# Kernel tuning notes

Measured on AMD Instinct MI355X. Metric: run time of the kernel, lower is better.

The kernel has to match this reference:

```python
import jax, jax.numpy as jnp
import numpy as np

H, W = 101, 31
HEADS, DH, FREQ = 8, 64, 64
C_DIM = 256
INNER = HEADS * DH
EPS = 1e-5


def _conv2d(x, w, b):
    # x: (B, Cin, H, W), w: (Cout, Cin, 3, 3) -> SAME padding, stride 1
    y = jax.lax.conv_general_dilated(x, w, (1, 1), 'SAME',
                                     dimension_numbers=('NCHW', 'OIHW', 'NCHW'))
    return y + b[None, :, None, None]


def setup_inputs() -> dict:
    key = jax.random.key(0)
    ks = jax.random.split(key, 8)
    B = 32
    N = H * W  # 3131
    s = 0.02
    x = jax.random.normal(ks[0], (B, N, C_DIM), jnp.float32)
    conv_fx_w = jax.random.normal(ks[1], (INNER, C_DIM, 3, 3), jnp.float32) * s
    conv_fx_b = jnp.zeros((INNER,), jnp.float32)
    conv_x_w = jax.random.normal(ks[2], (INNER, C_DIM, 3, 3), jnp.float32) * s
    conv_x_b = jnp.zeros((INNER,), jnp.float32)
    gate_w = jax.random.normal(ks[3], (FREQ, DH), jnp.float32) * s  # nn.Linear weight (out,in)
    gate_b = jnp.zeros((FREQ,), jnp.float32)
    temperature = jnp.full((1, HEADS, 1, 1), 0.5, jnp.float32)
    ln_gamma = jnp.ones((FREQ, DH), jnp.float32)
    ln_beta = jnp.zeros((FREQ, DH), jnp.float32)
    mlp_w = jax.random.normal(ks[4], (DH, DH), jnp.float32) * s
    out_w = jax.random.normal(ks[5], (C_DIM, INNER), jnp.float32) * s
    out_b = jnp.zeros((C_DIM,), jnp.float32)
    # fixed (non-trainable) spectral basis, L2-normalized per row like F.normalize(dim=-1)
    inver = jax.random.normal(ks[6], (N, FREQ), jnp.float32)
    inver = inver / jnp.linalg.norm(inver, axis=-1, keepdims=True)
    return dict(x=x, conv_fx_w=conv_fx_w, conv_fx_b=conv_fx_b, conv_x_w=conv_x_w,
                conv_x_b=conv_x_b, gate_w=gate_w, gate_b=gate_b,
                temperature=temperature, ln_gamma=ln_gamma, ln_beta=ln_beta,
                mlp_w=mlp_w, out_w=out_w, out_b=out_b, inver=inver)


def reference(x, conv_fx_w, conv_fx_b, conv_x_w, conv_x_b, gate_w, gate_b,
              temperature, ln_gamma, ln_beta, mlp_w, out_w, out_b, inver):
    B, N, C = x.shape
    xi = x.reshape(B, H, W, C).transpose(0, 3, 1, 2)  # (B, C, H, W)

    def proj(w, b):
        y = _conv2d(xi, w, b)                                  # (B, inner, H, W)
        return y.transpose(0, 2, 3, 1).reshape(B, N, HEADS, DH).transpose(0, 2, 1, 3)  # (B,h,N,d)

    fx_mid = proj(conv_fx_w, conv_fx_b)
    x_mid = proj(conv_x_w, conv_x_b)

    temp = jnp.clip(temperature, 0.1, 5.0)                      # (1,h,1,1)
    logits = jnp.einsum('bhnc,gc->bhng', x_mid, gate_w) + gate_b
    gate = jax.nn.softmax(logits / temp, axis=-1)               # (B,h,N,g)
    eigens = gate * inver[None, None]                           # (B,h,N,g)

    spec = jnp.einsum('bhnc,bhng->bhgc', fx_mid, eigens)        # (B,h,g,c)
    # LayerNorm over the trailing (g, c) axes jointly
    mu = spec.mean(axis=(-2, -1), keepdims=True)
    var = spec.var(axis=(-2, -1), keepdims=True)
    spec = (spec - mu) * jax.lax.rsqrt(var + EPS) * ln_gamma + ln_beta

    out_spec = jnp.einsum('bhgi,io->bhgo', spec, mlp_w)
    out_x = jnp.einsum('bhgc,bhng->bhnc', out_spec, eigens)     # (B,h,N,c)
    out_x = out_x.transpose(0, 2, 1, 3).reshape(B, N, HEADS * DH)
    return jnp.einsum('bnd,cd->bnc', out_x, out_w) + out_b      # to_out (dropout is identity)
```

## Files before the change

kernel.cpp:

```cpp
#include <hip/hip_runtime.h>
#include <hip/hip_bf16.h>
#include <stdint.h>

#define HH 101
#define WW 31
#define NN 3131
#define NPAD 3136
#define BB 32
#define NH 8
#define CDIM 256
#define GG 64
#define HP 103
#define WP 33

typedef __attribute__((ext_vector_type(8))) short bf16x8;
typedef __attribute__((ext_vector_type(4))) float f32x4;
typedef __attribute__((ext_vector_type(4))) unsigned short ushort4_t;
typedef __attribute__((ext_vector_type(8))) unsigned short ushort8_t;
typedef __attribute__((ext_vector_type(4))) float float4_t;

static __device__ __forceinline__ unsigned short f2bf(float f) {
  union { float f; uint32_t u; } v; v.f = f;
  uint32_t u = v.u;
  return (unsigned short)((u + 0x7fffu + ((u >> 16) & 1u)) >> 16);
}
static __device__ __forceinline__ float bf2f(unsigned short h) {
  union { uint32_t u; float f; } v; v.u = ((uint32_t)h) << 16;
  return v.f;
}
static __device__ __forceinline__ void gload_lds16(const void* g, void* l) {
  __builtin_amdgcn_global_load_lds((const __attribute__((address_space(1))) void*)g,
                                   (__attribute__((address_space(3))) void*)l, 16, 0, 0);
}
static __device__ __forceinline__ int xcd_swz(int bid, int nwg) {
  int q = nwg >> 3, r = nwg & 7;
  int xcd = bid & 7, pos = bid >> 3;
  int base = (xcd < r) ? xcd * (q + 1) : r * (q + 1) + (xcd - r) * q;
  return base + pos;
}

__global__ void k_pad(const float* __restrict__ x, unsigned short* __restrict__ xpad, int b0) {
  const int xx = blockIdx.x, yy = blockIdx.y, b = blockIdx.z;
  const int t = threadIdx.x;
  ushort4_t o; o.x = 0; o.y = 0; o.z = 0; o.w = 0;
  if (yy >= 1 && yy <= HH && xx >= 1 && xx <= WW) {
    const int n = (yy - 1) * WW + (xx - 1);
    const float4_t v = *(const float4_t*)(x + (((int64_t)(b0 + b) * NN + n) * CDIM + t * 4));
    o.x = f2bf(v.x); o.y = f2bf(v.y); o.z = f2bf(v.z); o.w = f2bf(v.w);
  }
  *(ushort4_t*)(xpad + (((int64_t)b * HP + yy) * WP + xx) * CDIM + t * 4) = o;
}

__global__ void k_wpack(const float* __restrict__ fxw, const float* __restrict__ xw,
                        const float* __restrict__ fxb, const float* __restrict__ xb,
                        const float* __restrict__ gw,
                        unsigned short* __restrict__ Wb, float* __restrict__ bias,
                        unsigned short* __restrict__ gwb) {
  int tid = blockIdx.x * blockDim.x + threadIdx.x;
  const int total = 9 * 1024 * 256;
  if (tid < total) {
    int cin = tid & 255; int rest = tid >> 8; int co = rest & 1023; int t = rest >> 10;
    float v = (co < 512) ? fxw[(int64_t)co * 2304 + cin * 9 + t]
                         : xw[(int64_t)(co - 512) * 2304 + cin * 9 + t];
    Wb[tid] = f2bf(v);
  }
  if (tid < 1024) bias[tid] = (tid < 512) ? fxb[tid] : xb[tid - 512];
  if (tid < 4096) gwb[tid] = f2bf(gw[tid]);
}

__global__ void k_pprep(const float* __restrict__ mlp, const float* __restrict__ outw,
                        unsigned short* __restrict__ Pt) {
  int h = blockIdx.x >> 6, i = blockIdx.x & 63, co = threadIdx.x;
  float a = 0.f;
  for (int c = 0; c < 64; ++c) a += mlp[i * 64 + c] * outw[(int64_t)co * 512 + h * 64 + c];
  Pt[((int64_t)h * 256 + co) * 64 + i] = f2bf(a);
}

__global__ void k_padzero(unsigned short* __restrict__ fxT, unsigned short* __restrict__ xmid,
                          int CB) {
  int tid = blockIdx.x * blockDim.x + threadIdx.x;
  if (tid >= CB * 2560) return;
  {
    int j = tid % 5; int rc = tid / 5;
    fxT[(int64_t)rc * NPAD + NN + j] = 0;
  }
  {
    int d = tid & 63; int rest = tid >> 6;
    int j = rest % 5; int bh = rest / 5;
    xmid[((int64_t)bh * NPAD + NN + j) * 64 + d] = 0;
  }
}

static __device__ __forceinline__ void stage_a8(const unsigned short* aS0, const unsigned short* aS1,
                                                unsigned short* lds, int s, int wid, int kt) {
  const int t = kt >> 3;
  const int dy = (t >= 6) + (t >= 3);
  const int dx = t - dy * 3;
  const int aoff = (dy * WP + dx) * CDIM + (kt & 7) * 32;
  gload_lds16(aS0 + aoff, lds + s * 16384 + wid * 512);
  gload_lds16(aS1 + aoff, lds + s * 16384 + 4096 + wid * 512);
}
static __device__ __forceinline__ void stage_b8(const unsigned short* bS0, const unsigned short* bS1,
                                                unsigned short* lds, int s, int wid, int kt) {
  const int t = kt >> 3;
  const int boff = t * (1024 * CDIM) + (kt & 7) * 32;
  gload_lds16(bS0 + boff, lds + s * 16384 + 8192 + wid * 512);
  gload_lds16(bS1 + boff, lds + s * 16384 + 8192 + 4096 + wid * 512);
}

__launch_bounds__(512, 2)
__global__ void k_conv8(const unsigned short* __restrict__ xpad,
                        const unsigned short* __restrict__ Wb,
                        const float* __restrict__ bias,
                        unsigned short* __restrict__ fxT,
                        unsigned short* __restrict__ xmid) {
  extern __shared__ unsigned short lds[];
  const int swz = xcd_swz(blockIdx.x, gridDim.x);
  const int r   = swz % 52;
  const int b   = swz / 52;
  const int bx  = r & 3;
  const int mt  = r >> 2;
  const int tid = threadIdx.x, wid = tid >> 6, lane = tid & 63;
  const int wm = wid >> 2, wn = wid & 3;
  const int arow = lane & 15, col16 = lane >> 4;
  const int n00 = mt * 256, co00 = bx * 256;

  const int srow = wid * 16 + (lane >> 2);
  const int tc   = ((lane & 3) ^ ((srow ^ (srow >> 2)) & 3)) * 8;
  int na0 = n00 + srow;        if (na0 >= NN) na0 = NN - 1;
  int na1 = n00 + srow + 128;  if (na1 >= NN) na1 = NN - 1;
  const int y0 = na0 / WW, x0v = na0 % WW;
  const int y1 = na1 / WW, x1v = na1 % WW;
  const unsigned short* aS0 = xpad + ((int64_t)(b * HP + y0) * WP + x0v) * CDIM + tc;
  const unsigned short* aS1 = xpad + ((int64_t)(b * HP + y1) * WP + x1v) * CDIM + tc;
  const unsigned short* bS0 = Wb + (int64_t)(co00 + srow) * CDIM + tc;
  const unsigned short* bS1 = Wb + (int64_t)(co00 + srow + 128) * CDIM + tc;

  const int rdcol = (col16 ^ ((arow ^ (arow >> 2)) & 3)) * 8;

  f32x4 acc[8][4] = {};

  stage_a8(aS0, aS1, lds, 0, wid, 0); stage_b8(bS0, bS1, lds, 0, wid, 0);
  stage_a8(aS0, aS1, lds, 1, wid, 1); stage_b8(bS0, bS1, lds, 1, wid, 1);

  for (int kt = 0; kt < 72; ++kt) {
    const int s = kt & 3;
    const unsigned short* sA = lds + s * 16384;
    const unsigned short* sB = sA + 8192;
    const int s2  = (kt + 2) & 3;
    const int kt2 = (kt + 2 > 71) ? 71 : kt + 2;

    asm volatile("s_waitcnt vmcnt(4)" ::: "memory");
    __builtin_amdgcn_s_barrier();
    asm volatile("" ::: "memory");
    __builtin_amdgcn_sched_barrier(0);

    stage_a8(aS0, aS1, lds, s2, wid, kt2);
    stage_b8(bS0, bS1, lds, s2, wid, kt2);

    bf16x8 av[8], bv[4];
    #pragma unroll
    for (int mf = 0; mf < 8; ++mf)
      av[mf] = *(const bf16x8*)(sA + (wm * 128 + mf * 16 + arow) * 32 + rdcol);
    #pragma unroll
    for (int nf = 0; nf < 4; ++nf)
      bv[nf] = *(const bf16x8*)(sB + (wn * 64 + nf * 16 + arow) * 32 + rdcol);
    __builtin_amdgcn_s_setprio(1);
    #pragma unroll
    for (int mf = 0; mf < 8; ++mf)
      #pragma unroll
      for (int nf = 0; nf < 4; ++nf)
        acc[mf][nf] = __builtin_amdgcn_mfma_f32_16x16x32_bf16(av[mf], bv[nf], acc[mf][nf], 0, 0, 0);
    __builtin_amdgcn_s_setprio(0);
  }

  asm volatile("s_waitcnt vmcnt(0)" ::: "memory");

  const int rowoff = col16 * 4;
  #pragma unroll
  for (int mf = 0; mf < 8; ++mf) {
    const int nr = n00 + wm * 128 + mf * 16 + rowoff;
    #pragma unroll
    for (int nf = 0; nf < 4; ++nf) {
      const int co = co00 + wn * 64 + nf * 16 + arow;
      const float bvs = bias[co];
      const float v0 = acc[mf][nf][0] + bvs;
      const float v1 = acc[mf][nf][1] + bvs;
      const float v2 = acc[mf][nf][2] + bvs;
      const float v3 = acc[mf][nf][3] + bvs;
      if (bx < 2) {
        const int h = co >> 6, c = co & 63;
        unsigned short* dst = fxT + ((int64_t)((b * NH + h) * 64 + c)) * NPAD + nr;
        if (nr + 3 < NN) {
          ushort4_t o; o.x = f2bf(v0); o.y = f2bf(v1); o.z = f2bf(v2); o.w = f2bf(v3);
          *(ushort4_t*)dst = o;
        } else {
          if (nr + 0 < NN) dst[0] = f2bf(v0);
          if (nr + 1 < NN) dst[1] = f2bf(v1);
          if (nr + 2 < NN) dst[2] = f2bf(v2);
          if (nr + 3 < NN) dst[3] = f2bf(v3);
        }
      } else {
        const int h = (co >> 6) & 7, d = co & 63;
        unsigned short* dst = xmid + ((int64_t)(b * NH + h) * NPAD + nr) * 64 + d;
        if (nr + 0 < NN) dst[0] = f2bf(v0);
        if (nr + 1 < NN) dst[64] = f2bf(v1);
        if (nr + 2 < NN) dst[128] = f2bf(v2);
        if (nr + 3 < NN) dst[192] = f2bf(v3);
      }
    }
  }
}

__global__ void k_eig(const unsigned short* __restrict__ xmid,
                      const unsigned short* __restrict__ gwb,
                      const float* __restrict__ gateb,
                      const float* __restrict__ temperature,
                      const float* __restrict__ inver,
                      unsigned short* __restrict__ eigT,
                      unsigned short* __restrict__ eigN) {
  __shared__ unsigned short egN[64 * 72];
  __shared__ unsigned short egT[64 * 72];
  const int nt = blockIdx.x, h = blockIdx.y, b = blockIdx.z;
  const int tid = threadIdx.x;
  const int w = tid >> 6, lane = tid & 63;
  const int n0 = nt * 64 + w * 16;
  const int bh = b * NH + h;
  float tv = temperature[h];
  tv = fminf(fmaxf(tv, 0.1f), 5.0f);
  const float itemp = 1.0f / tv;
  const int arow = lane & 15;
  const int koff = (lane >> 4) * 8;
  const unsigned short* aptr = xmid + ((int64_t)bh * NPAD + (n0 + arow)) * 64 + koff;
  bf16x8 a0 = *(const bf16x8*)(aptr);
  bf16x8 a1 = *(const bf16x8*)(aptr + 32);
  f32x4 acc[4] = {};
  #pragma unroll
  for (int ng = 0; ng < 4; ++ng) {
    const unsigned short* bptr = gwb + (ng * 16 + arow) * 64 + koff;
    bf16x8 b0 = *(const bf16x8*)(bptr);
    bf16x8 b1 = *(const bf16x8*)(bptr + 32);
    acc[ng] = __builtin_amdgcn_mfma_f32_16x16x32_bf16(a0, b0, acc[ng], 0, 0, 0);
    acc[ng] = __builtin_amdgcn_mfma_f32_16x16x32_bf16(a1, b1, acc[ng], 0, 0, 0);
  }
  #pragma unroll
  for (int r = 0; r < 4; ++r) {
    const int nl = w * 16 + ((lane >> 4) << 2) + r;
    const int n = nt * 64 + nl;
    float vals[4];
    #pragma unroll
    for (int ng = 0; ng < 4; ++ng) vals[ng] = (acc[ng][r] + gateb[ng * 16 + arow]) * itemp;
    float mx = fmaxf(fmaxf(vals[0], vals[1]), fmaxf(vals[2], vals[3]));
    #pragma unroll
    for (int s = 1; s < 16; s <<= 1) mx = fmaxf(mx, __shfl_xor(mx, s));
    float ex[4]; float sum = 0.f;
    #pragma unroll
    for (int ng = 0; ng < 4; ++ng) { ex[ng] = __expf(vals[ng] - mx); sum += ex[ng]; }
    #pragma unroll
    for (int s = 1; s < 16; s <<= 1) sum += __shfl_xor(sum, s);
    const float inv = 1.0f / sum;
    const bool valid = (n < NN);
    #pragma unroll
    for (int ng = 0; ng < 4; ++ng) {
      const int g = ng * 16 + arow;
      float iv = valid ? inver[(int64_t)n * GG + g] : 0.f;
      unsigned short u = valid ? f2bf(ex[ng] * inv * iv) : (unsigned short)0;
      egN[nl * 72 + g] = u;
      egT[g * 72 + nl] = u;
    }
  }
  __syncthreads();
  const int row = tid >> 2, c0 = (tid & 3) << 4;
  {
    ushort8_t v0 = *(ushort8_t*)&egN[row * 72 + c0];
    ushort8_t v1 = *(ushort8_t*)&egN[row * 72 + c0 + 8];
    unsigned short* dst = eigN + ((int64_t)bh * NPAD + nt * 64 + row) * 64 + c0;
    *(ushort8_t*)dst = v0; *(ushort8_t*)(dst + 8) = v1;
  }
  {
    ushort8_t v0 = *(ushort8_t*)&egT[row * 72 + c0];
    ushort8_t v1 = *(ushort8_t*)&egT[row * 72 + c0 + 8];
    unsigned short* dst = eigT + ((int64_t)(bh * 64 + row)) * NPAD + nt * 64 + c0;
    *(ushort8_t*)dst = v0; *(ushort8_t*)(dst + 8) = v1;
  }
}

__launch_bounds__(256, 1)
__global__ void k_specln(const unsigned short* __restrict__ eigT,
                         const unsigned short* __restrict__ fxT,
                         const float* __restrict__ gamma, const float* __restrict__ beta,
                         const unsigned short* __restrict__ Pt,
                         unsigned short* __restrict__ m2t) {
  extern __shared__ char sm[];
  float* sacc = (float*)sm;
  unsigned short* specb = (unsigned short*)(sm + 66560);
  float* red = (float*)(sm + 74752);
  unsigned short* mstrip = (unsigned short*)(sm + 74784);
  const int bhl = blockIdx.x;
  const int h = bhl & 7, bl = bhl >> 3;
  const int tid = threadIdx.x, w = tid >> 6, lane = tid & 63;
  const int arow = lane & 15, col16 = lane >> 4;
  const int koff = col16 * 8;
  const unsigned short* eb = eigT + (int64_t)bhl * 64 * NPAD;
  const unsigned short* fb = fxT + (int64_t)bhl * 64 * NPAD;

  const int ks0 = (98 * w) >> 2, ks1 = (98 * (w + 1)) >> 2;
  f32x4 acc[4][4] = {};
  for (int ks = ks0; ks < ks1; ++ks) {
    const int k0 = ks * 32 + koff;
    bf16x8 av[4], bv[4];
    #pragma unroll
    for (int mg = 0; mg < 4; ++mg) av[mg] = *(const bf16x8*)(eb + (int64_t)(mg * 16 + arow) * NPAD + k0);
    #pragma unroll
    for (int ng = 0; ng < 4; ++ng) bv[ng] = *(const bf16x8*)(fb + (int64_t)(ng * 16 + arow) * NPAD + k0);
    #pragma unroll
    for (int mg = 0; mg < 4; ++mg)
      #pragma unroll
      for (int ng = 0; ng < 4; ++ng)
        acc[mg][ng] = __builtin_amdgcn_mfma_f32_16x16x32_bf16(av[mg], bv[ng], acc[mg][ng], 0, 0, 0);
  }
  float* pw = sacc + w * (64 * 65);
  #pragma unroll
  for (int mg = 0; mg < 4; ++mg)
    #pragma unroll
    for (int ng = 0; ng < 4; ++ng)
      #pragma unroll
      for (int r = 0; r < 4; ++r)
        pw[(mg * 16 + col16 * 4 + r) * 65 + ng * 16 + arow] = acc[mg][ng][r];
  __syncthreads();

  float vloc[16];
  float lsum = 0.f, lsq = 0.f;
  #pragma unroll
  for (int idx = 0; idx < 16; ++idx) {
    const int e = tid + idx * 256;
    const int g = e >> 6, c = e & 63;
    float v = sacc[g * 65 + c] + sacc[4160 + g * 65 + c] +
              sacc[8320 + g * 65 + c] + sacc[12480 + g * 65 + c];
    vloc[idx] = v; lsum += v; lsq += v * v;
  }
  #pragma unroll
  for (int s = 1; s < 64; s <<= 1) { lsum += __shfl_xor(lsum, s); lsq += __shfl_xor(lsq, s); }
  if (lane == 0) { red[w] = lsum; red[4 + w] = lsq; }
  __syncthreads();
  const float tsum = red[0] + red[1] + red[2] + red[3];
  const float tsq = red[4] + red[5] + red[6] + red[7];
  const float mu = tsum * (1.0f / 4096.0f);
  const float var = tsq * (1.0f / 4096.0f) - mu * mu;
  const float rs = rsqrtf(var + 1e-5f);
  #pragma unroll
  for (int idx = 0; idx < 16; ++idx) {
    const int e = tid + idx * 256;
    const int g = e >> 6, c = e & 63;
    float sv = (vloc[idx] - mu) * rs * gamma[e] + beta[e];
    specb[g * 64 + ((((c >> 3) ^ (g & 7))) << 3) + (c & 7)] = f2bf(sv);
  }
  __syncthreads();

  f32x4 a2[4][4] = {};
  const unsigned short* pth = Pt + ((int64_t)h * 256 + w * 64) * 64;
  #pragma unroll
  for (int kk = 0; kk < 2; ++kk) {
    const int i0 = kk * 32 + koff;
    const int i8 = (i0 >> 3);
    bf16x8 av2[4], bv2[4];
    #pragma unroll
    for (int mg = 0; mg < 4; ++mg) {
      const int g = mg * 16 + arow;
      av2[mg] = *(const bf16x8*)(specb + g * 64 + ((i8 ^ (g & 7)) << 3));
    }
    #pragma unroll
    for (int ng = 0; ng < 4; ++ng)
      bv2[ng] = *(const bf16x8*)(pth + (ng * 16 + arow) * 64 + i0);
    #pragma unroll
    for (int mg = 0; mg < 4; ++mg)
      #pragma unroll
      for (int ng = 0; ng < 4; ++ng)
        a2[mg][ng] = __builtin_amdgcn_mfma_f32_16x16x32_bf16(av2[mg], bv2[ng], a2[mg][ng], 0, 0, 0);
  }
  unsigned short* ms = mstrip + w * (64 * 72);
  #pragma unroll
  for (int mg = 0; mg < 4; ++mg)
    #pragma unroll
    for (int ng = 0; ng < 4; ++ng)
      #pragma unroll
      for (int r = 0; r < 4; ++r)
        ms[(ng * 16 + arow) * 72 + mg * 16 + col16 * 4 + r] = f2bf(a2[mg][ng][r]);
  __syncthreads();
  #pragma unroll
  for (int e0 = 0; e0 < 8; ++e0) {
    const int e = lane + e0 * 64;
    const int row = e >> 3, g8 = e & 7;
    ushort8_t v = *(ushort8_t*)&ms[row * 72 + g8 * 8];
    *(ushort8_t*)(m2t + ((int64_t)(bl * 256 + w * 64 + row)) * 512 + h * 64 + g8 * 8) = v;
  }
}

__launch_bounds__(256)
__global__ void k_out(const unsigned short* __restrict__ eigN,
                      const unsigned short* __restrict__ m2t,
                      const float* __restrict__ outb,
                      float* __restrict__ out, int b0) {
  const int swz = xcd_swz(blockIdx.x, gridDim.x);
  const int ct = swz & 1;
  const int mt = (swz >> 1) % 25;
  const int b  = swz / 50;
  const int w = threadIdx.x >> 6, lane = threadIdx.x & 63;
  const int wm = w >> 1, wn = w & 1;
  const int arow = lane & 15, koff = (lane >> 4) * 8;
  const int co0 = ct * 128 + wn * 64;
  const int n0 = mt * 128 + wm * 64;
  f32x4 acc[4][4] = {};
  const unsigned short* ebase = eigN + (int64_t)b * NH * NPAD * 64;
  const unsigned short* mbase = m2t + (int64_t)b * 256 * 512;
  for (int ks = 0; ks < 16; ++ks) {
    const int hh = ks >> 1;
    const int g0 = (ks & 1) * 32 + koff;
    bf16x8 av[4], bv[4];
    #pragma unroll
    for (int mg = 0; mg < 4; ++mg) {
      int n = n0 + mg * 16 + arow;
      if (n > NPAD - 1) n = NPAD - 1;
      av[mg] = *(const bf16x8*)(ebase + ((int64_t)hh * NPAD + n) * 64 + g0);
    }
    #pragma unroll
    for (int ng = 0; ng < 4; ++ng)
      bv[ng] = *(const bf16x8*)(mbase + (int64_t)(co0 + ng * 16 + arow) * 512 + ks * 32 + koff);
    #pragma unroll
    for (int mg = 0; mg < 4; ++mg)
      #pragma unroll
      for (int ng = 0; ng < 4; ++ng)
        acc[mg][ng] = __builtin_amdgcn_mfma_f32_16x16x32_bf16(av[mg], bv[ng], acc[mg][ng], 0, 0, 0);
  }
  #pragma unroll
  for (int mg = 0; mg < 4; ++mg) {
    const int nr = n0 + mg * 16 + ((lane >> 4) << 2);
    #pragma unroll
    for (int ng = 0; ng < 4; ++ng) {
      const int co = co0 + ng * 16 + arow;
      const float bv = outb[co];
      #pragma unroll
      for (int r = 0; r < 4; ++r) {
        if (nr + r < NN)
          out[((int64_t)(b0 + b) * NN + nr + r) * 256 + co] = acc[mg][ng][r] + bv;
      }
    }
  }
}

extern "C" void kernel_launch(void* const* d_in, const int* in_sizes, int n_in,
                              void* d_out, int out_size, void* d_ws, size_t ws_size,
                              hipStream_t stream) {
  const float* x     = (const float*)d_in[0];
  const float* fxw   = (const float*)d_in[1];
  const float* fxb   = (const float*)d_in[2];
  const float* xw    = (const float*)d_in[3];
  const float* xb    = (const float*)d_in[4];
  const float* gw    = (const float*)d_in[5];
  const float* gb    = (const float*)d_in[6];
  const float* temp  = (const float*)d_in[7];
  const float* gamma = (const float*)d_in[8];
  const float* beta  = (const float*)d_in[9];
  const float* mlp   = (const float*)d_in[10];
  const float* outw  = (const float*)d_in[11];
  const float* outb  = (const float*)d_in[12];
  const float* inver = (const float*)d_in[13];
  float* out = (float*)d_out;
  char* ws = (char*)d_ws;
  (void)in_sizes; (void)n_in; (void)out_size;

  hipFuncSetAttribute(reinterpret_cast<const void*>(k_conv8),
                      hipFuncAttributeMaxDynamicSharedMemorySize, 131072);
  hipFuncSetAttribute(reinterpret_cast<const void*>(k_specln),
                      hipFuncAttributeMaxDynamicSharedMemorySize, 131072);

  int CB = 1;
  {
    const int cands[6] = {32, 16, 8, 4, 2, 1};
    for (int i = 0; i < 6; ++i) {
      unsigned long long need = 4993024ull + (unsigned long long)cands[i] * 14847488ull;
      if (need <= (unsigned long long)ws_size) { CB = cands[i]; break; }
    }
  }

  unsigned short* Wb   = (unsigned short*)(ws + 0);
  float*          bias = (float*)(ws + 4718592);
  unsigned short* gwb  = (unsigned short*)(ws + 4722688);
  unsigned short* Pt   = (unsigned short*)(ws + 4730880);
  const size_t F0      = 4993024;
  const size_t szXpad  = (size_t)CB * 1740288;
  const size_t szM2t   = (size_t)CB * 262144;
  const size_t szBig   = (size_t)CB * 3211264;
  unsigned short* xpad = (unsigned short*)(ws + F0);
  unsigned short* m2t  = (unsigned short*)(ws + F0 + szXpad);
  unsigned short* fxT  = (unsigned short*)(ws + F0 + szXpad + szM2t);
  unsigned short* xmid = (unsigned short*)(ws + F0 + szXpad + szM2t + szBig);
  unsigned short* eigT = (unsigned short*)(ws + F0 + szXpad + szM2t + 2 * szBig);
  unsigned short* eigN = (unsigned short*)(ws + F0 + szXpad + szM2t + 3 * szBig);

  k_wpack<<<dim3(9216), dim3(256), 0, stream>>>(fxw, xw, fxb, xb, gw, Wb, bias, gwb);
  k_pprep<<<dim3(512), dim3(256), 0, stream>>>(mlp, outw, Pt);

  for (int b0 = 0; b0 < BB; b0 += CB) {
    k_pad<<<dim3(WP, HP, CB), dim3(64), 0, stream>>>(x, xpad, b0);
    k_padzero<<<dim3(CB * 10), dim3(256), 0, stream>>>(fxT, xmid, CB);
    k_conv8<<<dim3(52 * CB), dim3(512), 131072, stream>>>(xpad, Wb, bias, fxT, xmid);
    k_eig<<<dim3(49, 8, CB), dim3(256), 0, stream>>>(xmid, gwb, gb, temp, inver, eigT, eigN);
    k_specln<<<dim3(CB * 8), dim3(256), 111648, stream>>>(eigT, fxT, gamma, beta, Pt, m2t);
    k_out<<<dim3(50 * CB), dim3(256), 0, stream>>>(eigN, m2t, outb, out, b0);
  }
}
```

Measured before the change: 930.1 us.

## Restructure conv GEMM main loop into double-buffered 64-wide K steps with interleaved phases

Rewrites the implicit-GEMM conv main loop from a 4-stage ring of 32-wide K tiles into a 2-buffer scheme where each iteration covers 64 K elements, split into four phases that interleave LDS reads, global-to-LDS prefetch of the next tile, barriers and MFMA pairs. The LDS swizzle pattern also changes. The aim is to cut barrier count per K element and to overlap memory prefetch with MFMA work more finely in a ping-pong style. In exchange, the per-buffer LDS footprint and barrier count per iteration go up, and the new swizzle may be less effective at avoiding bank conflicts.

```diff
diff --git a/kernel.cpp b/kernel.cpp
--- a/kernel.cpp
+++ b/kernel.cpp
@@ -89,23 +89,6 @@
     int j = rest % 5; int bh = rest / 5;
     xmid[((int64_t)bh * NPAD + NN + j) * 64 + d] = 0;
   }
-}
-
-static __device__ __forceinline__ void stage_a8(const unsigned short* aS0, const unsigned short* aS1,
-                                                unsigned short* lds, int s, int wid, int kt) {
-  const int t = kt >> 3;
-  const int dy = (t >= 6) + (t >= 3);
-  const int dx = t - dy * 3;
-  const int aoff = (dy * WP + dx) * CDIM + (kt & 7) * 32;
-  gload_lds16(aS0 + aoff, lds + s * 16384 + wid * 512);
-  gload_lds16(aS1 + aoff, lds + s * 16384 + 4096 + wid * 512);
-}
-static __device__ __forceinline__ void stage_b8(const unsigned short* bS0, const unsigned short* bS1,
-                                                unsigned short* lds, int s, int wid, int kt) {
-  const int t = kt >> 3;
-  const int boff = t * (1024 * CDIM) + (kt & 7) * 32;
-  gload_lds16(bS0 + boff, lds + s * 16384 + 8192 + wid * 512);
-  gload_lds16(bS1 + boff, lds + s * 16384 + 8192 + 4096 + wid * 512);
 }
 
 __launch_bounds__(512, 2)
@@ -126,7 +109,7 @@
   const int n00 = mt * 256, co00 = bx * 256;
 
   const int srow = wid * 16 + (lane >> 2);
-  const int tc   = ((lane & 3) ^ ((srow ^ (srow >> 2)) & 3)) * 8;
+  const int tc   = ((lane & 3) ^ ((lane >> 3) & 3)) * 8;
   int na0 = n00 + srow;        if (na0 >= NN) na0 = NN - 1;
   int na1 = n00 + srow + 128;  if (na1 >= NN) na1 = NN - 1;
   const int y0 = na0 / WW, x0v = na0 % WW;
@@ -136,42 +119,96 @@
   const unsigned short* bS0 = Wb + (int64_t)(co00 + srow) * CDIM + tc;
   const unsigned short* bS1 = Wb + (int64_t)(co00 + srow + 128) * CDIM + tc;
 
-  const int rdcol = (col16 ^ ((arow ^ (arow >> 2)) & 3)) * 8;
+  const int rdsz = (col16 ^ ((arow >> 1) & 3)) * 8;
 
   f32x4 acc[8][4] = {};
 
-  stage_a8(aS0, aS1, lds, 0, wid, 0); stage_b8(bS0, bS1, lds, 0, wid, 0);
-  stage_a8(aS0, aS1, lds, 1, wid, 1); stage_b8(bS0, bS1, lds, 1, wid, 1);
-
-  for (int kt = 0; kt < 72; ++kt) {
-    const int s = kt & 3;
-    const unsigned short* sA = lds + s * 16384;
-    const unsigned short* sB = sA + 8192;
-    const int s2  = (kt + 2) & 3;
-    const int kt2 = (kt + 2 > 71) ? 71 : kt + 2;
-
+#define STAGE_A(s, kk, aoffv)                                        \
+  { unsigned short* d = lds + (s) * 32768 + (kk) * 8192 + wid * 512; \
+    gload_lds16(aS0 + (aoffv) + (kk) * 32, d);                       \
+    gload_lds16(aS1 + (aoffv) + (kk) * 32, d + 4096); }
+#define STAGE_B(s, kk, boffv)                                                \
+  { unsigned short* d = lds + (s) * 32768 + 16384 + (kk) * 8192 + wid * 512; \
+    gload_lds16(bS0 + (boffv) + (kk) * 32, d);                               \
+    gload_lds16(bS1 + (boffv) + (kk) * 32, d + 4096); }
+#define KOFF(ks, aoffv, boffv)                              \
+  { const int tap = (ks) >> 2;                              \
+    const int dy = (tap >= 6) + (tap >= 3);                 \
+    const int dx = tap - dy * 3;                            \
+    const int cb = ((ks) & 3) << 6;                         \
+    aoffv = (dy * WP + dx) * CDIM + cb;                     \
+    boffv = tap * 262144 + cb; }
+
+  int aoff0, boff0;
+  KOFF(0, aoff0, boff0);
+  STAGE_A(0, 0, aoff0); STAGE_B(0, 0, boff0);
+  STAGE_A(0, 1, aoff0); STAGE_B(0, 1, boff0);
+  asm volatile("s_waitcnt vmcnt(4)" ::: "memory");
+  __builtin_amdgcn_s_barrier();
+  asm volatile("" ::: "memory");
+
+#define MFMA_PAIR(n0i, n1i)                                                              \
+  __builtin_amdgcn_s_setprio(1);                                                        \
+  _Pragma("unroll")                                                                      \
+  for (int mf = 0; mf < 8; ++mf) {                                                       \
+    acc[mf][n0i] = __builtin_amdgcn_mfma_f32_16x16x32_bf16(av[mf], bv0, acc[mf][n0i], 0, 0, 0); \
+    acc[mf][n1i] = __builtin_amdgcn_mfma_f32_16x16x32_bf16(av[mf], bv1, acc[mf][n1i], 0, 0, 0); \
+  }                                                                                      \
+  __builtin_amdgcn_s_setprio(0);
+#define BAR_PRE()                                              \
+  __builtin_amdgcn_s_barrier();                                \
+  asm volatile("s_waitcnt lgkmcnt(0)" ::: "memory");           \
+  __builtin_amdgcn_sched_barrier(0);
+#define BAR_POST()                                             \
+  asm volatile("" ::: "memory");                               \
+  __builtin_amdgcn_s_barrier();                                \
+  asm volatile("" ::: "memory");
+
+  #pragma unroll 1
+  for (int t = 0; t < 36; ++t) {
+    const int cur = t & 1, nxt = cur ^ 1;
+    const int tn = (t < 35) ? t + 1 : 35;
+    int aoffn, boffn;
+    KOFF(tn, aoffn, boffn);
+    unsigned short* sA0 = lds + cur * 32768;
+    unsigned short* sB0 = sA0 + 16384;
+    bf16x8 av[8], bv0, bv1;
+
+    #pragma unroll
+    for (int mf = 0; mf < 8; ++mf)
+      av[mf] = *(const bf16x8*)(sA0 + (wm * 128 + mf * 16 + arow) * 32 + rdsz);
+    bv0 = *(const bf16x8*)(sB0 + (wn * 64 + 0 + arow) * 32 + rdsz);
+    bv1 = *(const bf16x8*)(sB0 + (wn * 64 + 16 + arow) * 32 + rdsz);
+    STAGE_A(nxt, 0, aoffn);
+    BAR_PRE();
+    MFMA_PAIR(0, 1);
+    BAR_POST();
+
+    bv0 = *(const bf16x8*)(sB0 + (wn * 64 + 32 + arow) * 32 + rdsz);
+    bv1 = *(const bf16x8*)(sB0 + (wn * 64 + 48 + arow) * 32 + rdsz);
+    STAGE_B(nxt, 0, boffn);
     asm volatile("s_waitcnt vmcnt(4)" ::: "memory");
-    __builtin_amdgcn_s_barrier();
-    asm volatile("" ::: "memory");
-    __builtin_amdgcn_sched_barrier(0);
-
-    stage_a8(aS0, aS1, lds, s2, wid, kt2);
-    stage_b8(bS0, bS1, lds, s2, wid, kt2);
-
-    bf16x8 av[8], bv[4];
+    BAR_PRE();
+    MFMA_PAIR(2, 3);
+    BAR_POST();
+
     #pragma unroll
     for (int mf = 0; mf < 8; ++mf)
-      av[mf] = *(const bf16x8*)(sA + (wm * 128 + mf * 16 + arow) * 32 + rdcol);
-    #pragma unroll
-    for (int nf = 0; nf < 4; ++nf)
-      bv[nf] = *(const bf16x8*)(sB + (wn * 64 + nf * 16 + arow) * 32 + rdcol);
-    __builtin_amdgcn_s_setprio(1);
-    #pragma unroll
-    for (int mf = 0; mf < 8; ++mf)
-      #pragma unroll
-      for (int nf = 0; nf < 4; ++nf)
-        acc[mf][nf] = __builtin_amdgcn_mfma_f32_16x16x32_bf16(av[mf], bv[nf], acc[mf][nf], 0, 0, 0);
-    __builtin_amdgcn_s_setprio(0);
+      av[mf] = *(const bf16x8*)(sA0 + 8192 + (wm * 128 + mf * 16 + arow) * 32 + rdsz);
+    bv0 = *(const bf16x8*)(sB0 + 8192 + (wn * 64 + 0 + arow) * 32 + rdsz);
+    bv1 = *(const bf16x8*)(sB0 + 8192 + (wn * 64 + 16 + arow) * 32 + rdsz);
+    STAGE_A(nxt, 1, aoffn);
+    BAR_PRE();
+    MFMA_PAIR(0, 1);
+    BAR_POST();
+
+    bv0 = *(const bf16x8*)(sB0 + 8192 + (wn * 64 + 32 + arow) * 32 + rdsz);
+    bv1 = *(const bf16x8*)(sB0 + 8192 + (wn * 64 + 48 + arow) * 32 + rdsz);
+    STAGE_B(nxt, 1, boffn);
+    asm volatile("s_waitcnt vmcnt(4)" ::: "memory");
+    BAR_PRE();
+    MFMA_PAIR(2, 3);
+    BAR_POST();
   }
 
   asm volatile("s_waitcnt vmcnt(0)" ::: "memory");
@@ -210,6 +247,12 @@
       }
     }
   }
+#undef STAGE_A
+#undef STAGE_B
+#undef KOFF
+#undef MFMA_PAIR
+#undef BAR_PRE
+#undef BAR_POST
 }
 
 __global__ void k_eig(const unsigned short* __restrict__ xmid,
```

Measured after the change: 905.6 us. 2.6% less time.

## Retile conv implicit GEMM to 128x256 tiles with 4 waves and triple-buffered LDS

Applied to the files above, without the earlier changes.

The conv kernel moves from 512-thread blocks with 256x256 output tiles and a 4-stage LDS ring to 256-thread blocks with 128x256 tiles and a 3-stage ring. The LDS swizzle and wait/barrier placement change to match. The grid grows from 52 to 100 blocks per batch, which fills the CUs better and wastes less on the partial last M tile, but each block reuses less data. The batch chunk size is also capped at 16 instead of 32, so the pipeline loop runs more times and issues more launches.

```diff
diff --git a/kernel.cpp b/kernel.cpp
--- a/kernel.cpp
+++ b/kernel.cpp
@@ -91,24 +91,7 @@
   }
 }
 
-static __device__ __forceinline__ void stage_a8(const unsigned short* aS0, const unsigned short* aS1,
-                                                unsigned short* lds, int s, int wid, int kt) {
-  const int t = kt >> 3;
-  const int dy = (t >= 6) + (t >= 3);
-  const int dx = t - dy * 3;
-  const int aoff = (dy * WP + dx) * CDIM + (kt & 7) * 32;
-  gload_lds16(aS0 + aoff, lds + s * 16384 + wid * 512);
-  gload_lds16(aS1 + aoff, lds + s * 16384 + 4096 + wid * 512);
-}
-static __device__ __forceinline__ void stage_b8(const unsigned short* bS0, const unsigned short* bS1,
-                                                unsigned short* lds, int s, int wid, int kt) {
-  const int t = kt >> 3;
-  const int boff = t * (1024 * CDIM) + (kt & 7) * 32;
-  gload_lds16(bS0 + boff, lds + s * 16384 + 8192 + wid * 512);
-  gload_lds16(bS1 + boff, lds + s * 16384 + 8192 + 4096 + wid * 512);
-}
-
-__launch_bounds__(512, 2)
+__launch_bounds__(256, 2)
 __global__ void k_conv8(const unsigned short* __restrict__ xpad,
                         const unsigned short* __restrict__ Wb,
                         const float* __restrict__ bias,
@@ -116,73 +99,106 @@
                         unsigned short* __restrict__ xmid) {
   extern __shared__ unsigned short lds[];
   const int swz = xcd_swz(blockIdx.x, gridDim.x);
-  const int r   = swz % 52;
-  const int b   = swz / 52;
+  const int r   = swz % 100;
+  const int b   = swz / 100;
   const int bx  = r & 3;
   const int mt  = r >> 2;
   const int tid = threadIdx.x, wid = tid >> 6, lane = tid & 63;
-  const int wm = wid >> 2, wn = wid & 3;
+  const int wm = wid >> 1, wn = wid & 1;
   const int arow = lane & 15, col16 = lane >> 4;
-  const int n00 = mt * 256, co00 = bx * 256;
-
-  const int srow = wid * 16 + (lane >> 2);
-  const int tc   = ((lane & 3) ^ ((srow ^ (srow >> 2)) & 3)) * 8;
-  int na0 = n00 + srow;        if (na0 >= NN) na0 = NN - 1;
-  int na1 = n00 + srow + 128;  if (na1 >= NN) na1 = NN - 1;
-  const int y0 = na0 / WW, x0v = na0 % WW;
-  const int y1 = na1 / WW, x1v = na1 % WW;
-  const unsigned short* aS0 = xpad + ((int64_t)(b * HP + y0) * WP + x0v) * CDIM + tc;
-  const unsigned short* aS1 = xpad + ((int64_t)(b * HP + y1) * WP + x1v) * CDIM + tc;
-  const unsigned short* bS0 = Wb + (int64_t)(co00 + srow) * CDIM + tc;
-  const unsigned short* bS1 = Wb + (int64_t)(co00 + srow + 128) * CDIM + tc;
-
-  const int rdcol = (col16 ^ ((arow ^ (arow >> 2)) & 3)) * 8;
-
-  f32x4 acc[8][4] = {};
-
-  stage_a8(aS0, aS1, lds, 0, wid, 0); stage_b8(bS0, bS1, lds, 0, wid, 0);
-  stage_a8(aS0, aS1, lds, 1, wid, 1); stage_b8(bS0, bS1, lds, 1, wid, 1);
-
-  for (int kt = 0; kt < 72; ++kt) {
-    const int s = kt & 3;
-    const unsigned short* sA = lds + s * 16384;
-    const unsigned short* sB = sA + 8192;
-    const int s2  = (kt + 2) & 3;
-    const int kt2 = (kt + 2 > 71) ? 71 : kt + 2;
-
-    asm volatile("s_waitcnt vmcnt(4)" ::: "memory");
+  const int n00 = mt * 128, co00 = bx * 256;
+
+  const int tc = ((lane & 3) ^ ((lane >> 3) & 3)) * 8;
+  const unsigned short* aS[2];
+  #pragma unroll
+  for (int i = 0; i < 2; ++i) {
+    const int srow = (wid * 2 + i) * 16 + (lane >> 2);
+    int na = n00 + srow; if (na >= NN) na = NN - 1;
+    const int y = na / WW, xv = na % WW;
+    aS[i] = xpad + ((int64_t)(b * HP + y) * WP + xv) * CDIM + tc;
+  }
+  const unsigned short* bS[4];
+  #pragma unroll
+  for (int i = 0; i < 4; ++i) {
+    const int srow = (wid * 4 + i) * 16 + (lane >> 2);
+    bS[i] = Wb + (int64_t)(co00 + srow) * CDIM + tc;
+  }
+
+  const int rdsz = (col16 ^ ((arow >> 1) & 3)) * 8;
+
+  f32x4 acc[4][8] = {};
+
+#define STAGE(s, aoffv, boffv)                                        \
+  { unsigned short* dA = lds + (s) * 12288 + wid * 1024;              \
+    gload_lds16(aS[0] + (aoffv), dA);                                 \
+    gload_lds16(aS[1] + (aoffv), dA + 512);                           \
+    unsigned short* dB = lds + (s) * 12288 + 4096 + wid * 2048;       \
+    gload_lds16(bS[0] + (boffv), dB);                                 \
+    gload_lds16(bS[1] + (boffv), dB + 512);                           \
+    gload_lds16(bS[2] + (boffv), dB + 1024);                          \
+    gload_lds16(bS[3] + (boffv), dB + 1536); }
+#define KOFF(ks, aoffv, boffv)                              \
+  { const int tap = (ks) >> 3;                              \
+    const int dy = (tap >= 6) + (tap >= 3);                 \
+    const int dx = tap - dy * 3;                            \
+    const int cb = ((ks) & 7) << 5;                         \
+    aoffv = (dy * WP + dx) * CDIM + cb;                     \
+    boffv = tap * 262144 + cb; }
+
+  {
+    int a0o, b0o, a1o, b1o;
+    KOFF(0, a0o, b0o); KOFF(1, a1o, b1o);
+    STAGE(0, a0o, b0o);
+    STAGE(1, a1o, b1o);
+  }
+  asm volatile("s_waitcnt vmcnt(6)" ::: "memory");
+  __builtin_amdgcn_s_barrier();
+  asm volatile("" ::: "memory");
+
+  #pragma unroll 1
+  for (int t = 0; t < 72; ++t) {
+    const int cur = t % 3;
+    const int s2  = (t + 2) % 3;
+    const int tn  = (t + 2 > 71) ? 71 : t + 2;
+    int aoffn, boffn;
+    KOFF(tn, aoffn, boffn);
+
+    STAGE(s2, aoffn, boffn);
+
+    const unsigned short* sA = lds + cur * 12288;
+    const unsigned short* sB = sA + 4096;
+    bf16x8 av[4], bv[8];
+    #pragma unroll
+    for (int mf = 0; mf < 4; ++mf)
+      av[mf] = *(const bf16x8*)(sA + (wm * 64 + mf * 16 + arow) * 32 + rdsz);
+    #pragma unroll
+    for (int nf = 0; nf < 8; ++nf)
+      bv[nf] = *(const bf16x8*)(sB + (wn * 128 + nf * 16 + arow) * 32 + rdsz);
+    asm volatile("s_waitcnt lgkmcnt(0)" ::: "memory");
+    __builtin_amdgcn_sched_barrier(0);
+
+    __builtin_amdgcn_s_setprio(1);
+    #pragma unroll
+    for (int mf = 0; mf < 4; ++mf)
+      #pragma unroll
+      for (int nf = 0; nf < 8; ++nf)
+        acc[mf][nf] = __builtin_amdgcn_mfma_f32_16x16x32_bf16(av[mf], bv[nf], acc[mf][nf], 0, 0, 0);
+    __builtin_amdgcn_s_setprio(0);
+
+    asm volatile("s_waitcnt vmcnt(6)" ::: "memory");
     __builtin_amdgcn_s_barrier();
     asm volatile("" ::: "memory");
-    __builtin_amdgcn_sched_barrier(0);
-
-    stage_a8(aS0, aS1, lds, s2, wid, kt2);
-    stage_b8(bS0, bS1, lds, s2, wid, kt2);
-
-    bf16x8 av[8], bv[4];
-    #pragma unroll
-    for (int mf = 0; mf < 8; ++mf)
-      av[mf] = *(const bf16x8*)(sA + (wm * 128 + mf * 16 + arow) * 32 + rdcol);
-    #pragma unroll
-    for (int nf = 0; nf < 4; ++nf)
-      bv[nf] = *(const bf16x8*)(sB + (wn * 64 + nf * 16 + arow) * 32 + rdcol);
-    __builtin_amdgcn_s_setprio(1);
-    #pragma unroll
-    for (int mf = 0; mf < 8; ++mf)
-      #pragma unroll
-      for (int nf = 0; nf < 4; ++nf)
-        acc[mf][nf] = __builtin_amdgcn_mfma_f32_16x16x32_bf16(av[mf], bv[nf], acc[mf][nf], 0, 0, 0);
-    __builtin_amdgcn_s_setprio(0);
-  }
-
-  asm volatile("s_waitcnt vmcnt(0)" ::: "memory");
+  }
+
+  asm volatile("s_waitcnt vmcnt(0) lgkmcnt(0)" ::: "memory");
 
   const int rowoff = col16 * 4;
   #pragma unroll
-  for (int mf = 0; mf < 8; ++mf) {
-    const int nr = n00 + wm * 128 + mf * 16 + rowoff;
-    #pragma unroll
-    for (int nf = 0; nf < 4; ++nf) {
-      const int co = co00 + wn * 64 + nf * 16 + arow;
+  for (int mf = 0; mf < 4; ++mf) {
+    const int nr = n00 + wm * 64 + mf * 16 + rowoff;
+    #pragma unroll
+    for (int nf = 0; nf < 8; ++nf) {
+      const int co = co00 + wn * 128 + nf * 16 + arow;
       const float bvs = bias[co];
       const float v0 = acc[mf][nf][0] + bvs;
       const float v1 = acc[mf][nf][1] + bvs;
@@ -210,6 +226,8 @@
       }
     }
   }
+#undef STAGE
+#undef KOFF
 }
 
 __global__ void k_eig(const unsigned short* __restrict__ xmid,
@@ -470,14 +488,14 @@
   (void)in_sizes; (void)n_in; (void)out_size;
 
   hipFuncSetAttribute(reinterpret_cast<const void*>(k_conv8),
-                      hipFuncAttributeMaxDynamicSharedMemorySize, 131072);
+                      hipFuncAttributeMaxDynamicSharedMemorySize, 73728);
   hipFuncSetAttribute(reinterpret_cast<const void*>(k_specln),
                       hipFuncAttributeMaxDynamicSharedMemorySize, 131072);
 
   int CB = 1;
   {
-    const int cands[6] = {32, 16, 8, 4, 2, 1};
-    for (int i = 0; i < 6; ++i) {
+    const int cands[5] = {16, 8, 4, 2, 1};
+    for (int i = 0; i < 5; ++i) {
       unsigned long long need = 4993024ull + (unsigned long long)cands[i] * 14847488ull;
       if (need <= (unsigned long long)ws_size) { CB = cands[i]; break; }
     }
@@ -504,7 +522,7 @@
   for (int b0 = 0; b0 < BB; b0 += CB) {
     k_pad<<<dim3(WP, HP, CB), dim3(64), 0, stream>>>(x, xpad, b0);
     k_padzero<<<dim3(CB * 10), dim3(256), 0, stream>>>(fxT, xmid, CB);
-    k_conv8<<<dim3(52 * CB), dim3(512), 131072, stream>>>(xpad, Wb, bias, fxT, xmid);
+    k_conv8<<<dim3(100 * CB), dim3(256), 73728, stream>>>(xpad, Wb, bias, fxT, xmid);
     k_eig<<<dim3(49, 8, CB), dim3(256), 0, stream>>>(xmid, gwb, gb, temp, inver, eigT, eigN);
     k_specln<<<dim3(CB * 8), dim3(256), 111648, stream>>>(eigT, fxT, gamma, beta, Pt, m2t);
     k_out<<<dim3(50 * CB), dim3(256), 0, stream>>>(eigN, m2t, outb, out, b0);
```

Measured after the change: 904.3 us. 2.8% less time.
